# Kernel tuning notes

Hardware: AMD Instinct MI355X
Metric: run time of the kernel (lower is better)

## Reference

```python
import jax, jax.numpy as jnp
import numpy as np

B, T, DIM = 4, 2048, 1024
H, DH = 16, 64  # num_heads, dim_head; weight_dim = H*DH = 1024
SCALE = DIM ** (-0.5)  # note: original scales by dim**-0.5, not dim_head**-0.5


def setup_inputs() -> dict:
    key = jax.random.key(0)
    k1, k2, k3 = jax.random.split(key, 3)
    x = jax.random.normal(k1, (B, T, DIM), dtype=jnp.float32)
    w_qkv = jax.random.normal(k2, (3 * H * DH, DIM), dtype=jnp.float32) * (DIM ** -0.5)
    w_out = jax.random.normal(k3, (DIM, H * DH), dtype=jnp.float32) * ((H * DH) ** -0.5)
    b_out = jnp.zeros((DIM,), dtype=jnp.float32)
    return {"x": x, "w_qkv": w_qkv, "w_out": w_out, "b_out": b_out}


def reference(x, w_qkv, w_out, b_out):
    # qkv: [b, t, 3*H*DH] (torch Linear: x @ W^T)
    qkv = jnp.einsum('btc,oc->bto', x, w_qkv)
    # rearrange 'b t (d k h) -> k b h t d' with k=3, h=H: d is the OUTERMOST
    # factor of the flattened axis, then k, then h (h fastest-varying).
    qkv = qkv.reshape(B, T, DH, 3, H)          # [b, t, d, k, h]
    qkv = jnp.transpose(qkv, (3, 0, 4, 1, 2))   # [k, b, h, t, d]
    q, k, v = qkv[0], qkv[1], qkv[2]
    # scores: [b, h, t, t]
    attn = jnp.einsum('bhid,bhjd->bhij', q, k) * SCALE
    attn = jax.nn.softmax(attn, axis=-1)
    out = jnp.einsum('bhij,bhjd->bhid', attn, v)           # [b, h, t, d]
    out = jnp.transpose(out, (0, 2, 1, 3)).reshape(B, T, H * DH)  # 'b h t d -> b t (h d)'
    return jnp.einsum('btc,oc->bto', out, w_out) + b_out
```

## Files before the change

### kernel.cpp

```cpp
#include <hip/hip_runtime.h>
#include <hip/hip_bf16.h>


typedef __attribute__((ext_vector_type(8))) short short8;
typedef __attribute__((ext_vector_type(4))) float floatx4;
typedef __attribute__((ext_vector_type(16))) float floatx16;

static __device__ __forceinline__ floatx4 mfma16(short8 a, short8 b, floatx4 c) {
    return __builtin_amdgcn_mfma_f32_16x16x32_bf16(a, b, c, 0, 0, 0);
}
static __device__ __forceinline__ floatx16 mfma32(short8 a, short8 b, floatx16 c) {
    return __builtin_amdgcn_mfma_f32_32x32x16_bf16(a, b, c, 0, 0, 0);
}

static __device__ __forceinline__ unsigned short f2bf_bits(float f) {
    __hip_bfloat16 h = __float2bfloat16(f);
    return *reinterpret_cast<unsigned short*>(&h);
}

static __device__ __forceinline__ float fast_exp2(float x) {
#if __has_builtin(__builtin_amdgcn_exp2f)
    return __builtin_amdgcn_exp2f(x);
#else
    return exp2f(x);
#endif
}

static __device__ __forceinline__ unsigned cvt_pk_bf16(float lo, float hi) {
    unsigned r;
    asm("v_cvt_pk_bf16_f32 %0, %1, %2" : "=v"(r) : "v"(lo), "v"(hi));
    return r;
}

static __device__ __forceinline__ void plane32_swap(unsigned& x, unsigned& y) {
#if __has_builtin(__builtin_amdgcn_permlane32_swap)
    typedef unsigned int uintx2 __attribute__((ext_vector_type(2)));
    uintx2 r = __builtin_amdgcn_permlane32_swap(x, y, false, false);
    x = r[0];
    y = r[1];
#else
    asm volatile("v_permlane32_swap_b32 %0, %1" : "+v"(x), "+v"(y));
#endif
}

#define GLD16(gptr, ldsptr)                                                  \
    __builtin_amdgcn_global_load_lds(                                        \
        (const __attribute__((address_space(1))) void*)(gptr),               \
        (__attribute__((address_space(3))) void*)(ldsptr), 16, 0, 0)

__global__ __launch_bounds__(256) void k_cvt(
    const float* __restrict__ src, unsigned short* __restrict__ dst, int n4)
{
    typedef __attribute__((ext_vector_type(4))) unsigned short ushort4v;
    for (int i = blockIdx.x * blockDim.x + threadIdx.x; i < n4;
         i += gridDim.x * blockDim.x) {
        const float4 v = ((const float4*)src)[i];
        ushort4v o;
        o.x = f2bf_bits(v.x);
        o.y = f2bf_bits(v.y);
        o.z = f2bf_bits(v.z);
        o.w = f2bf_bits(v.w);
        ((ushort4v*)dst)[i] = o;
    }
}

__global__ __launch_bounds__(256) void k_qkv(
    const unsigned short* __restrict__ x,
    const unsigned short* __restrict__ wq,
    unsigned short* __restrict__ qb,
    unsigned short* __restrict__ kb,
    unsigned short* __restrict__ vb)
{
    __shared__ unsigned short SM[16384];

    const int tid  = threadIdx.x;
    const int wave = tid >> 6, lane = tid & 63;
    const int quad = lane >> 4, l16 = lane & 15;
    const int wm = wave >> 1, wn = wave & 1;

    const int fid  = blockIdx.y * 24 + blockIdx.x;
    const int nfid = (fid & 7) * 192 + (fid >> 3);
    const int bx = nfid % 24;
    const int m0 = (nfid / 24) * 128;
    const int kk = bx >> 3;
    const int cb = bx & 7;

    const int srow = lane >> 2;
    const int sc8  = (lane & 3) * 8;
    const int row0 = wave * 32 + srow;
    const int row1 = row0 + 16;
    int bn0, bn1;
    if (kk < 2) {
        bn0 = (row0 & 63) * 48 + kk * 16 + cb * 2 + (row0 >> 6);
        bn1 = (row1 & 63) * 48 + kk * 16 + cb * 2 + (row1 >> 6);
    } else {
        bn0 = (cb * 8 + (row0 >> 4)) * 48 + 32 + (row0 & 15);
        bn1 = (cb * 8 + (row1 >> 4)) * 48 + 32 + (row1 & 15);
    }

    floatx4 acc[4][4];
#pragma unroll
    for (int i = 0; i < 4; i++)
#pragma unroll
        for (int j = 0; j < 4; j++) acc[i][j] = (floatx4){0.f, 0.f, 0.f, 0.f};

#define QKV_STAGE(BUF, K0)                                                        \
    do {                                                                          \
        GLD16(&x[(m0 + row0) * 1024 + (K0) + sc8],                                \
              &SM[(BUF) * 8192 + (wave * 32) * 32]);                              \
        GLD16(&x[(m0 + row1) * 1024 + (K0) + sc8],                                \
              &SM[(BUF) * 8192 + (wave * 32 + 16) * 32]);                         \
        GLD16(&wq[bn0 * 1024 + (K0) + sc8],                                       \
              &SM[(BUF) * 8192 + 4096 + (wave * 32) * 32]);                       \
        GLD16(&wq[bn1 * 1024 + (K0) + sc8],                                       \
              &SM[(BUF) * 8192 + 4096 + (wave * 32 + 16) * 32]);                  \
    } while (0)

    QKV_STAGE(0, 0);
    int buf = 0;
    for (int k0 = 0; k0 < 1024; k0 += 32) {
        __syncthreads();
        if (k0 + 32 < 1024) QKV_STAGE(buf ^ 1, k0 + 32);

        const unsigned short* Ab = &SM[buf * 8192];
        const unsigned short* Bb = &SM[buf * 8192 + 4096];
        short8 af[4], bfv[4];
#pragma unroll
        for (int mi = 0; mi < 4; mi++)
            af[mi] = *(const short8*)&Ab[(wm * 64 + mi * 16 + l16) * 32 + quad * 8];
#pragma unroll
        for (int ni = 0; ni < 4; ni++)
            bfv[ni] = *(const short8*)&Bb[(wn * 64 + ni * 16 + l16) * 32 + quad * 8];
#pragma unroll
        for (int mi = 0; mi < 4; mi++)
#pragma unroll
            for (int ni = 0; ni < 4; ni++)
                acc[mi][ni] = mfma16(af[mi], bfv[ni], acc[mi][ni]);
        buf ^= 1;
    }
    __syncthreads();

    if (kk == 2) {
#pragma unroll
        for (int ni = 0; ni < 4; ni++) {
            const int d = cb * 8 + wn * 4 + ni;
#pragma unroll
            for (int mi = 0; mi < 4; mi++) {
                const int m  = m0 + wm * 64 + mi * 16 + quad * 4;
                const int b  = m >> 11;
                const int tt = m & 2047;
                ushort4 pk;
                pk.x = f2bf_bits(acc[mi][ni][0]);
                pk.y = f2bf_bits(acc[mi][ni][1]);
                pk.z = f2bf_bits(acc[mi][ni][2]);
                pk.w = f2bf_bits(acc[mi][ni][3]);
                *(ushort4*)&vb[((b * 16 + l16) * 64 + d) * 2048 + tt] = pk;
            }
        }
    } else {
        const float scale = (kk == 0) ? 0.045084220027780106f : 1.0f;
        unsigned short* dst = (kk == 0) ? qb : kb;
        const int b = m0 >> 11, tt0 = m0 & 2047;
#pragma unroll
        for (int s = 0; s < 2; s++) {
            if (wn == s) {
#pragma unroll
                for (int ni = 0; ni < 4; ni++) {
                    const int d = ni * 16 + l16;
#pragma unroll
                    for (int mi = 0; mi < 4; mi++) {
                        const int tl = wm * 64 + mi * 16 + quad * 4;
#pragma unroll
                        for (int r = 0; r < 4; r++)
                            SM[(tl + r) * 72 + d] = f2bf_bits(acc[mi][ni][r] * scale);
                    }
                }
            }
            __syncthreads();
#pragma unroll
            for (int u = 0; u < 4; u++) {
                const int w  = tid + u * 256;
                const int tl = w >> 3;
                const int ch = (w & 7) * 8;
                *(uint4*)&dst[((b * 16 + cb * 2 + s) * 2048 + tt0 + tl) * 64 + ch] =
                    *(const uint4*)&SM[tl * 72 + ch];
            }
            __syncthreads();
        }
    }
#undef QKV_STAGE
}

__global__ __launch_bounds__(256, 2) void k_attn(
    const unsigned short* __restrict__ qt,
    const unsigned short* __restrict__ kt,
    const unsigned short* __restrict__ vg,
    __hip_bfloat16* __restrict__ og)
{
    const int tid  = threadIdx.x;
    const int wave = tid >> 6, lane = tid & 63;
    const int l31  = lane & 31, hi = lane >> 5;
    const int blk = blockIdx.x;
    const int bh  = (blk & 7) | ((blk >> 6) << 3);
    const int q0  = ((blk >> 3) & 7) * 256;
    const int qr  = q0 + wave * 64;

    short8 qf[2][4];
#pragma unroll
    for (int qb2 = 0; qb2 < 2; qb2++)
#pragma unroll
        for (int ks = 0; ks < 4; ks++)
            qf[qb2][ks] = *(const short8*)
                &qt[(bh * 2048 + qr + qb2 * 32 + l31) * 64 + ks * 16 + hi * 8];

    float lsum[2] = {0.f, 0.f};
    floatx16 o[2][2];
#pragma unroll
    for (int qb2 = 0; qb2 < 2; qb2++)
#pragma unroll
        for (int db = 0; db < 2; db++)
#pragma unroll
            for (int r = 0; r < 16; r++) o[qb2][db][r] = 0.f;

    const unsigned short* kbase = &kt[bh * 2048 * 64];
    const unsigned short* vbase = &vg[bh * 64 * 2048];

#pragma unroll 2
    for (int j = 0; j < 2048; j += 32) {
        short8 kf[4];
#pragma unroll
        for (int ks = 0; ks < 4; ks++)
            kf[ks] = *(const short8*)&kbase[(j + l31) * 64 + ks * 16 + hi * 8];

        floatx16 st[2];
#pragma unroll
        for (int qb2 = 0; qb2 < 2; qb2++)
#pragma unroll
            for (int r = 0; r < 16; r++) st[qb2][r] = 0.f;
        __builtin_amdgcn_s_setprio(1);
#pragma unroll
        for (int ks = 0; ks < 4; ks++)
#pragma unroll
            for (int qb2 = 0; qb2 < 2; qb2++)
                st[qb2] = mfma32(kf[ks], qf[qb2][ks], st[qb2]);
        __builtin_amdgcn_s_setprio(0);

        short8 vf[2][2];
#pragma unroll
        for (int db = 0; db < 2; db++)
#pragma unroll
            for (int hf = 0; hf < 2; hf++)
                vf[db][hf] = *(const short8*)
                    &vbase[(db * 32 + l31) * 2048 + j + hf * 16 + hi * 8];

        short8 paf[2][2];
#pragma unroll
        for (int qb2 = 0; qb2 < 2; qb2++) {
            float p[16];
#pragma unroll
            for (int r = 0; r < 16; r++) p[r] = fast_exp2(st[qb2][r]);
            lsum[qb2] += (((p[0] + p[1]) + (p[2] + p[3])) +
                          ((p[4] + p[5]) + (p[6] + p[7]))) +
                         (((p[8] + p[9]) + (p[10] + p[11])) +
                          ((p[12] + p[13]) + (p[14] + p[15])));
#pragma unroll
            for (int hf = 0; hf < 2; hf++) {
                const int r0 = hf * 8;
                unsigned c01 = cvt_pk_bf16(p[r0 + 0], p[r0 + 1]);
                unsigned c23 = cvt_pk_bf16(p[r0 + 2], p[r0 + 3]);
                unsigned c45 = cvt_pk_bf16(p[r0 + 4], p[r0 + 5]);
                unsigned c67 = cvt_pk_bf16(p[r0 + 6], p[r0 + 7]);
                plane32_swap(c01, c45);
                plane32_swap(c23, c67);
                uint4 t4 = {c01, c23, c45, c67};
                paf[qb2][hf] = *reinterpret_cast<short8*>(&t4);
            }
        }

        __builtin_amdgcn_s_setprio(1);
#pragma unroll
        for (int qb2 = 0; qb2 < 2; qb2++)
#pragma unroll
            for (int db = 0; db < 2; db++)
#pragma unroll
                for (int hf = 0; hf < 2; hf++)
                    o[qb2][db] = mfma32(paf[qb2][hf], vf[db][hf], o[qb2][db]);
        __builtin_amdgcn_s_setprio(0);
    }

    lsum[0] += __shfl_xor(lsum[0], 32);
    lsum[1] += __shfl_xor(lsum[1], 32);

    const int b = bh >> 4, h = bh & 15;
#pragma unroll
    for (int qb2 = 0; qb2 < 2; qb2++) {
#pragma unroll
        for (int r = 0; r < 16; r++) {
            const int qrl = (r & 3) + 8 * (r >> 2) + 4 * hi;
            const float inv = 1.0f / __shfl(lsum[qb2], qrl);
            const int t = qr + qb2 * 32 + qrl;
#pragma unroll
            for (int db = 0; db < 2; db++)
                og[(b * 2048 + t) * 1024 + h * 64 + db * 32 + l31] =
                    __float2bfloat16(o[qb2][db][r] * inv);
        }
    }
}

__global__ __launch_bounds__(256) void k_out(
    const unsigned short* __restrict__ a,
    const unsigned short* __restrict__ wq,
    const float* __restrict__ bias,
    float* __restrict__ out)
{
    __shared__ unsigned short SM[16384];

    const int tid  = threadIdx.x;
    const int wave = tid >> 6, lane = tid & 63;
    const int quad = lane >> 4, l16 = lane & 15;
    const int wm = wave >> 1, wn = wave & 1;

    const int fid  = blockIdx.y * 8 + blockIdx.x;
    const int nfid = (fid & 7) * 64 + (fid >> 3);
    const int n0 = (nfid & 7) * 128;
    const int m0 = (nfid >> 3) * 128;

    const int srow = lane >> 2;
    const int sc8  = (lane & 3) * 8;
    const int row0 = wave * 32 + srow;
    const int row1 = row0 + 16;

    floatx4 acc[4][4];
#pragma unroll
    for (int i = 0; i < 4; i++)
#pragma unroll
        for (int j = 0; j < 4; j++) acc[i][j] = (floatx4){0.f, 0.f, 0.f, 0.f};

#define OUT_STAGE(BUF, K0)                                                        \
    do {                                                                          \
        GLD16(&a[(m0 + row0) * 1024 + (K0) + sc8],                                \
              &SM[(BUF) * 8192 + (wave * 32) * 32]);                              \
        GLD16(&a[(m0 + row1) * 1024 + (K0) + sc8],                                \
              &SM[(BUF) * 8192 + (wave * 32 + 16) * 32]);                         \
        GLD16(&wq[(n0 + row0) * 1024 + (K0) + sc8],                               \
              &SM[(BUF) * 8192 + 4096 + (wave * 32) * 32]);                       \
        GLD16(&wq[(n0 + row1) * 1024 + (K0) + sc8],                               \
              &SM[(BUF) * 8192 + 4096 + (wave * 32 + 16) * 32]);                  \
    } while (0)

    OUT_STAGE(0, 0);
    int buf = 0;
    for (int k0 = 0; k0 < 1024; k0 += 32) {
        __syncthreads();
        if (k0 + 32 < 1024) OUT_STAGE(buf ^ 1, k0 + 32);

        const unsigned short* Ab = &SM[buf * 8192];
        const unsigned short* Bb = &SM[buf * 8192 + 4096];
        short8 af[4], bfv[4];
#pragma unroll
        for (int mi = 0; mi < 4; mi++)
            af[mi] = *(const short8*)&Ab[(wm * 64 + mi * 16 + l16) * 32 + quad * 8];
#pragma unroll
        for (int ni = 0; ni < 4; ni++)
            bfv[ni] = *(const short8*)&Bb[(wn * 64 + ni * 16 + l16) * 32 + quad * 8];
#pragma unroll
        for (int mi = 0; mi < 4; mi++)
#pragma unroll
            for (int ni = 0; ni < 4; ni++)
                acc[mi][ni] = mfma16(af[mi], bfv[ni], acc[mi][ni]);
        buf ^= 1;
    }
#undef OUT_STAGE

#pragma unroll
    for (int ni = 0; ni < 4; ni++) {
        const int col = n0 + wn * 64 + ni * 16 + l16;
        const float bv = bias[col];
#pragma unroll
        for (int mi = 0; mi < 4; mi++) {
            const int mbase = m0 + wm * 64 + mi * 16 + quad * 4;
#pragma unroll
            for (int r = 0; r < 4; r++)
                out[(mbase + r) * 1024 + col] = acc[mi][ni][r] + bv;
        }
    }
}

extern "C" void kernel_launch(void* const* d_in, const int* in_sizes, int n_in,
                              void* d_out, int out_size, void* d_ws, size_t ws_size,
                              hipStream_t stream) {
    const float* x    = (const float*)d_in[0];
    const float* wqkv = (const float*)d_in[1];
    const float* wout = (const float*)d_in[2];
    const float* bout = (const float*)d_in[3];
    float* out = (float*)d_out;

    unsigned short* ws = (unsigned short*)d_ws;
    unsigned short* xb    = ws;
    unsigned short* wqkvb = xb + 8388608;
    unsigned short* woutb = wqkvb + 3145728;
    unsigned short* qb    = woutb + 1048576;
    unsigned short* kb    = qb + 8388608;
    unsigned short* vb    = kb + 8388608;
    unsigned short* ob    = vb + 8388608;

    k_cvt<<<2048, 256, 0, stream>>>(x,    xb,    8388608 / 4);
    k_cvt<<<1024, 256, 0, stream>>>(wqkv, wqkvb, 3145728 / 4);
    k_cvt<<<512,  256, 0, stream>>>(wout, woutb, 1048576 / 4);

    k_qkv<<<dim3(24, 64), 256, 0, stream>>>(xb, wqkvb, qb, kb, vb);
    k_attn<<<512, 256, 0, stream>>>(qb, kb, vb, (__hip_bfloat16*)ob);
    k_out<<<dim3(8, 64), 256, 0, stream>>>(ob, woutb, bout, out);
}
```

Baseline: 312.1 us.

## Stage K/V tiles through LDS ring buffer and software-pipeline QK with softmax/PV

The attention kernel previously read K and V fragments straight from global memory in every iteration. It now stages 64-key K and V tiles into a four-deep padded LDS ring buffer, with register prefetch running a few tiles ahead. The QK^T of the next 32-key sub-block is interleaved with the exp/PV of the previous one, so MFMA work overlaps the softmax VALU work. This adds 72KB of LDS per block, which may limit occupancy under launch_bounds(256,2), and adds a barrier every iteration.

```diff
diff --git a/kernel.cpp b/kernel.cpp
--- a/kernel.cpp
+++ b/kernel.cpp
@@ -123,7 +123,7 @@
         if (k0 + 32 < 1024) QKV_STAGE(buf ^ 1, k0 + 32);
 
         const unsigned short* Ab = &SM[buf * 8192];
-        const unsigned short* Bb = &SM[buf * 8192 + 4096];
+        const unsigned short* Bb = Ab + 4096;
         short8 af[4], bfv[4];
 #pragma unroll
         for (int mi = 0; mi < 4; mi++)
@@ -197,6 +197,9 @@
     const unsigned short* __restrict__ vg,
     __hip_bfloat16* __restrict__ og)
 {
+    __shared__ unsigned short Ks[4 * 4608];
+    __shared__ unsigned short Vt[4 * 4608];
+
     const int tid  = threadIdx.x;
     const int wave = tid >> 6, lane = tid & 63;
     const int l31  = lane & 31, hi = lane >> 5;
@@ -222,71 +225,130 @@
 #pragma unroll
             for (int r = 0; r < 16; r++) o[qb2][db][r] = 0.f;
 
-    const unsigned short* kbase = &kt[bh * 2048 * 64];
-    const unsigned short* vbase = &vg[bh * 64 * 2048];
-
-#pragma unroll 2
-    for (int j = 0; j < 2048; j += 32) {
-        short8 kf[4];
-#pragma unroll
-        for (int ks = 0; ks < 4; ks++)
-            kf[ks] = *(const short8*)&kbase[(j + l31) * 64 + ks * 16 + hi * 8];
-
-        floatx16 st[2];
-#pragma unroll
-        for (int qb2 = 0; qb2 < 2; qb2++)
-#pragma unroll
-            for (int r = 0; r < 16; r++) st[qb2][r] = 0.f;
-        __builtin_amdgcn_s_setprio(1);
-#pragma unroll
-        for (int ks = 0; ks < 4; ks++)
-#pragma unroll
-            for (int qb2 = 0; qb2 < 2; qb2++)
-                st[qb2] = mfma32(kf[ks], qf[qb2][ks], st[qb2]);
-        __builtin_amdgcn_s_setprio(0);
-
-        short8 vf[2][2];
-#pragma unroll
-        for (int db = 0; db < 2; db++)
-#pragma unroll
-            for (int hf = 0; hf < 2; hf++)
-                vf[db][hf] = *(const short8*)
-                    &vbase[(db * 32 + l31) * 2048 + j + hf * 16 + hi * 8];
-
-        short8 paf[2][2];
-#pragma unroll
-        for (int qb2 = 0; qb2 < 2; qb2++) {
-            float p[16];
-#pragma unroll
-            for (int r = 0; r < 16; r++) p[r] = fast_exp2(st[qb2][r]);
-            lsum[qb2] += (((p[0] + p[1]) + (p[2] + p[3])) +
-                          ((p[4] + p[5]) + (p[6] + p[7]))) +
-                         (((p[8] + p[9]) + (p[10] + p[11])) +
-                          ((p[12] + p[13]) + (p[14] + p[15])));
-#pragma unroll
-            for (int hf = 0; hf < 2; hf++) {
-                const int r0 = hf * 8;
-                unsigned c01 = cvt_pk_bf16(p[r0 + 0], p[r0 + 1]);
-                unsigned c23 = cvt_pk_bf16(p[r0 + 2], p[r0 + 3]);
-                unsigned c45 = cvt_pk_bf16(p[r0 + 4], p[r0 + 5]);
-                unsigned c67 = cvt_pk_bf16(p[r0 + 6], p[r0 + 7]);
-                plane32_swap(c01, c45);
-                plane32_swap(c23, c67);
-                uint4 t4 = {c01, c23, c45, c67};
-                paf[qb2][hf] = *reinterpret_cast<short8*>(&t4);
-            }
-        }
-
-        __builtin_amdgcn_s_setprio(1);
-#pragma unroll
-        for (int qb2 = 0; qb2 < 2; qb2++)
-#pragma unroll
-            for (int db = 0; db < 2; db++)
-#pragma unroll
-                for (int hf = 0; hf < 2; hf++)
-                    o[qb2][db] = mfma32(paf[qb2][hf], vf[db][hf], o[qb2][db]);
-        __builtin_amdgcn_s_setprio(0);
-    }
+    const int sr = tid >> 2, sc = (tid & 3) * 16;
+    const unsigned short* kR = &kt[(bh * 2048 + sr) * 64 + sc];
+    const unsigned short* vR = &vg[(bh * 64 + sr) * 2048 + sc];
+
+    uint4 rka, rkb, rva, rvb;
+#define LOADT(T)                                                   \
+    do {                                                           \
+        rka = *(const uint4*)&kR[(T) * 4096];                      \
+        rkb = *(const uint4*)&kR[(T) * 4096 + 8];                  \
+        rva = *(const uint4*)&vR[(T) * 64];                        \
+        rvb = *(const uint4*)&vR[(T) * 64 + 8];                    \
+    } while (0)
+#define WRITET(B)                                                  \
+    do {                                                           \
+        *(uint4*)&Ks[(B) * 4608 + sr * 72 + sc]     = rka;         \
+        *(uint4*)&Ks[(B) * 4608 + sr * 72 + sc + 8] = rkb;         \
+        *(uint4*)&Vt[(B) * 4608 + sr * 72 + sc]     = rva;         \
+        *(uint4*)&Vt[(B) * 4608 + sr * 72 + sc + 8] = rvb;         \
+    } while (0)
+
+#define SOFTMAX(ST, PAF)                                                        \
+    do {                                                                        \
+        _Pragma("unroll")                                                       \
+        for (int qb2 = 0; qb2 < 2; qb2++) {                                     \
+            float p[16];                                                        \
+            _Pragma("unroll")                                                   \
+            for (int r = 0; r < 16; r++) p[r] = fast_exp2((ST)[qb2][r]);        \
+            lsum[qb2] += (((p[0] + p[1]) + (p[2] + p[3])) +                     \
+                          ((p[4] + p[5]) + (p[6] + p[7]))) +                    \
+                         (((p[8] + p[9]) + (p[10] + p[11])) +                   \
+                          ((p[12] + p[13]) + (p[14] + p[15])));                 \
+            _Pragma("unroll")                                                   \
+            for (int hf = 0; hf < 2; hf++) {                                    \
+                const int r0 = hf * 8;                                          \
+                unsigned c01 = cvt_pk_bf16(p[r0 + 0], p[r0 + 1]);               \
+                unsigned c23 = cvt_pk_bf16(p[r0 + 2], p[r0 + 3]);               \
+                unsigned c45 = cvt_pk_bf16(p[r0 + 4], p[r0 + 5]);               \
+                unsigned c67 = cvt_pk_bf16(p[r0 + 6], p[r0 + 7]);               \
+                plane32_swap(c01, c45);                                         \
+                plane32_swap(c23, c67);                                         \
+                uint4 t4 = {c01, c23, c45, c67};                                \
+                (PAF)[qb2][hf] = *reinterpret_cast<short8*>(&t4);               \
+            }                                                                   \
+        }                                                                       \
+    } while (0)
+
+#define PV(PAF, BO, KB2)                                                        \
+    do {                                                                        \
+        short8 vf[2][2];                                                        \
+        _Pragma("unroll")                                                       \
+        for (int db = 0; db < 2; db++)                                          \
+            _Pragma("unroll")                                                   \
+            for (int hf = 0; hf < 2; hf++)                                      \
+                vf[db][hf] = *(const short8*)&Vt[(BO) + (db * 32 + l31) * 72 +  \
+                                                 (KB2) * 32 + hf * 16 + hi * 8];\
+        __builtin_amdgcn_s_setprio(1);                                          \
+        _Pragma("unroll")                                                       \
+        for (int qb2 = 0; qb2 < 2; qb2++)                                       \
+            _Pragma("unroll")                                                   \
+            for (int db = 0; db < 2; db++)                                      \
+                _Pragma("unroll")                                               \
+                for (int hf = 0; hf < 2; hf++)                                  \
+                    o[qb2][db] = mfma32((PAF)[qb2][hf], vf[db][hf], o[qb2][db]);\
+        __builtin_amdgcn_s_setprio(0);                                          \
+    } while (0)
+
+#define QK(ST, BO, KB2)                                                         \
+    do {                                                                        \
+        short8 kf[4];                                                           \
+        _Pragma("unroll")                                                       \
+        for (int ks = 0; ks < 4; ks++)                                          \
+            kf[ks] = *(const short8*)&Ks[(BO) + ((KB2) * 32 + l31) * 72 +       \
+                                         ks * 16 + hi * 8];                     \
+        _Pragma("unroll")                                                       \
+        for (int qb2 = 0; qb2 < 2; qb2++)                                       \
+            _Pragma("unroll")                                                   \
+            for (int r = 0; r < 16; r++) (ST)[qb2][r] = 0.f;                    \
+        __builtin_amdgcn_s_setprio(1);                                          \
+        _Pragma("unroll")                                                       \
+        for (int ks = 0; ks < 4; ks++)                                          \
+            _Pragma("unroll")                                                   \
+            for (int qb2 = 0; qb2 < 2; qb2++)                                   \
+                (ST)[qb2] = mfma32(kf[ks], qf[qb2][ks], (ST)[qb2]);             \
+        __builtin_amdgcn_s_setprio(0);                                          \
+    } while (0)
+
+    LOADT(0);
+    WRITET(0);
+    LOADT(1);
+    WRITET(1);
+    LOADT(2);
+    asm volatile("s_waitcnt lgkmcnt(0)" ::: "memory");
+    __builtin_amdgcn_s_barrier();
+    __builtin_amdgcn_sched_barrier(0);
+
+    floatx16 stP[2];
+    QK(stP, 0, 0);
+
+    for (int j = 0; j < 32; ++j) {
+        const int bj  = (j & 3) * 4608;
+        const int bj1 = ((j + 1) & 3) * 4608;
+        if (j <= 29) WRITET((j + 2) & 3);
+        if (j <= 28) LOADT(j + 3);
+
+        floatx16 stN[2];
+        QK(stN, bj, 1);
+        short8 pafP[2][2];
+        SOFTMAX(stP, pafP);
+        PV(pafP, bj, 0);
+
+        if (j <= 30) QK(stP, bj1, 0);
+        short8 pafN[2][2];
+        SOFTMAX(stN, pafN);
+        PV(pafN, bj, 1);
+
+        asm volatile("s_waitcnt lgkmcnt(0)" ::: "memory");
+        __builtin_amdgcn_s_barrier();
+        __builtin_amdgcn_sched_barrier(0);
+    }
+#undef QK
+#undef PV
+#undef SOFTMAX
+#undef WRITET
+#undef LOADT
 
     lsum[0] += __shfl_xor(lsum[0], 32);
     lsum[1] += __shfl_xor(lsum[1], 32);
@@ -355,7 +417,7 @@
         if (k0 + 32 < 1024) OUT_STAGE(buf ^ 1, k0 + 32);
 
         const unsigned short* Ab = &SM[buf * 8192];
-        const unsigned short* Bb = &SM[buf * 8192 + 4096];
+        const unsigned short* Bb = Ab + 4096;
         short8 af[4], bfv[4];
 #pragma unroll
         for (int mi = 0; mi < 4; mi++)
```

Measured after the change: 260.4 us (median of 2 runs). -16.5%, faster.
